# Kernel optimization log

Measured on AMD Instinct MI355X. Metric: run time of the kernel, lower is better.

The kernel has to match this reference:

```python
import jax, jax.numpy as jnp
import numpy as np

SCALE_WEIGHT = 0.5 ** 0.5


def setup_inputs() -> dict:
    key = jax.random.key(0)
    ks = jax.random.split(key, 6)
    B, C, T, S = 8, 512, 2048, 2048
    base_target_emb = jax.random.normal(ks[0], (B, C, T, 1), dtype=jnp.float32)
    inp = jax.random.normal(ks[1], (B, C, T, 1), dtype=jnp.float32)
    encoder_out_t = jax.random.normal(ks[2], (B, C, S), dtype=jnp.float32)
    encoder_out_c = jax.random.normal(ks[3], (B, C, S), dtype=jnp.float32)
    # nn.Linear(input_size, input_size) params: W [out, in], b [out]
    bound = 1.0 / np.sqrt(C)
    W = jax.random.uniform(ks[4], (C, C), minval=-bound, maxval=bound, dtype=jnp.float32)
    b = jax.random.uniform(ks[5], (C,), minval=-bound, maxval=bound, dtype=jnp.float32)
    return {"base_target_emb": base_target_emb, "input": inp,
            "encoder_out_t": encoder_out_t, "encoder_out_c": encoder_out_c,
            "W": W, "b": b}


def reference(base_target_emb, input, encoder_out_t, encoder_out_c, W, b):
    # base_target_emb, input: [B, C, T, 1]; encoder_out_t/c: [B, C, S]
    x = input[..., 0]                                   # [B, C, T]
    # seq_linear: Linear over channel dim (y = W x + b)
    preatt = jnp.einsum('bct,oc->bot', x, W) + b[None, :, None]
    target = (base_target_emb[..., 0] + preatt) * SCALE_WEIGHT  # [B, C, T]
    # bmm(target^T, enc_t): scores over source positions
    pre_a = jnp.einsum('bct,bcs->bts', target, encoder_out_t)   # [B, T, S]
    attn = jax.nn.softmax(pre_a, axis=-1)                       # [B, T, S]
    # bmm(attn, enc_c^T): attention-weighted sum of values
    ctx = jnp.einsum('bts,bcs->btc', attn, encoder_out_c)       # [B, T, C]
    context_output = jnp.transpose(ctx, (0, 2, 1))[..., None]   # [B, C, T, 1]
    return context_output, attn
```

## Files before the change

### kernel.cpp

```cpp
#include <hip/hip_runtime.h>

typedef unsigned short u16;
typedef __attribute__((ext_vector_type(4))) float f4;
typedef __attribute__((ext_vector_type(8))) short bf8;
typedef __attribute__((ext_vector_type(8))) _Float16 h8;
typedef __attribute__((ext_vector_type(4))) unsigned short u16x4;

#define B_ 8
#define C_ 512
#define T_ 2048
#define S_ 2048
#define SCALE_W 0.70710678118654752440f

__device__ __forceinline__ u16 f2h(float f) {
  return __builtin_bit_cast(u16, (_Float16)f);
}
__device__ __forceinline__ float h2f(u16 h) {
  return (float)__builtin_bit_cast(_Float16, h);
}

__device__ __forceinline__ void gload16(const u16* g, u16* l) {
  __builtin_amdgcn_global_load_lds((__attribute__((address_space(1))) const void*)g,
                                   (__attribute__((address_space(3))) void*)l, 16, 0, 0);
}

#define MEMF() asm volatile("" ::: "memory")
#define BAR()  do { MEMF(); __builtin_amdgcn_s_barrier(); MEMF(); } while (0)
#define LGKM0() do { asm volatile("s_waitcnt lgkmcnt(0)" ::: "memory"); \
                     __builtin_amdgcn_sched_barrier(0); } while (0)

__global__ __launch_bounds__(256) void transpose_kernel(
    const float* __restrict__ in, u16* __restrict__ oh, int X)
{
  __shared__ float t[32][33];
  const int tx = threadIdx.x, ty = threadIdx.y;
  const long cbase = (long)blockIdx.z * C_ + blockIdx.y * 32;
  const long xbase = (long)blockIdx.x * 32;
  const float* ip = in + cbase * X + xbase;
#pragma unroll
  for (int i = 0; i < 4; ++i)
    t[ty + i * 8][tx] = ip[(long)(ty + i * 8) * X + tx];
  __syncthreads();
  const long obase = ((long)blockIdx.z * X + xbase) * C_ + blockIdx.y * 32;
#pragma unroll
  for (int i = 0; i < 4; ++i)
    oh[obase + (long)(ty + i * 8) * C_ + tx] = f2h(t[tx][ty + i * 8]);
}

template<int LO>
__global__ __launch_bounds__(256) void split_kernel(
    const float* __restrict__ in, u16* __restrict__ oh, u16* __restrict__ ol, long n4)
{
  long i = (long)blockIdx.x * 256 + threadIdx.x;
  const long stride = (long)gridDim.x * 256;
  for (; i < n4; i += stride) {
    f4 v = ((const f4*)in)[i];
    u16x4 hv, lv;
#pragma unroll
    for (int j = 0; j < 4; ++j) {
      u16 h = f2h(v[j]);
      hv[j] = h;
      if (LO) lv[j] = f2h(v[j] - h2f(h));
    }
    ((u16x4*)oh)[i] = hv;
    if (LO) ((u16x4*)ol)[i] = lv;
  }
}

__global__ __launch_bounds__(256, 2) void gemm1_kernel(
    const u16* __restrict__ A,
    const u16* __restrict__ Bh, const u16* __restrict__ Bl,
    const float* __restrict__ baseO, const float* __restrict__ bias,
    u16* __restrict__ outH, u16* __restrict__ outL)
{
  constexpr int BM = 128, BK = 32, K = C_, N = C_;
  constexpr int TILE = BM * BK;
  __shared__ u16 lA[TILE], lBh[TILE], lBl[TILE];

  const int tid = threadIdx.x;
  const int wid = tid >> 6;
  const int lane = tid & 63;
  const int wr = wid >> 1, wc = wid & 1;
  const int bz = blockIdx.z;
  const int m0 = blockIdx.y * BM;
  const int n0 = blockIdx.x * BM;

  const u16* gA  = A + ((long)bz * T_ + m0) * K;
  const u16* gBh = Bh + (long)n0 * K;
  const u16* gBl = Bl + (long)n0 * K;

  const int srow = tid >> 2;
  const int skoff = (tid & 3) * 8;
  const int ldsOff = wid * 512;

  f4 acc[4][4] = {};

  for (int k0 = 0; k0 < K; k0 += BK) {
    __syncthreads();
#pragma unroll
    for (int c = 0; c < 2; ++c) {
      const long go = (long)(c * 64 + srow) * K + k0 + skoff;
      const int lo = c * 2048 + ldsOff;
      gload16(gA + go, lA + lo);
      gload16(gBh + go, lBh + lo);
      gload16(gBl + go, lBl + lo);
    }
    asm volatile("s_waitcnt vmcnt(0)" ::: "memory");
    __syncthreads();

    bf8 a_[4], b_h[4], b_l[4];
    const int fr = lane & 15;
    const int fk = (lane >> 4) * 8;
#pragma unroll
    for (int i = 0; i < 4; ++i) {
      a_[i]  = *(const bf8*)&lA[(wr * 64 + i * 16 + fr) * BK + fk];
      b_h[i] = *(const bf8*)&lBh[(wc * 64 + i * 16 + fr) * BK + fk];
      b_l[i] = *(const bf8*)&lBl[(wc * 64 + i * 16 + fr) * BK + fk];
    }
#pragma unroll
    for (int mi = 0; mi < 4; ++mi)
#pragma unroll
      for (int ni = 0; ni < 4; ++ni) {
        acc[mi][ni] = __builtin_amdgcn_mfma_f32_16x16x32_f16(
            __builtin_bit_cast(h8, a_[mi]), __builtin_bit_cast(h8, b_h[ni]),
            acc[mi][ni], 0, 0, 0);
        acc[mi][ni] = __builtin_amdgcn_mfma_f32_16x16x32_f16(
            __builtin_bit_cast(h8, a_[mi]), __builtin_bit_cast(h8, b_l[ni]),
            acc[mi][ni], 0, 0, 0);
      }
  }

  const int fr = lane & 15;
  const int r4 = (lane >> 4) * 4;
#pragma unroll
  for (int mi = 0; mi < 4; ++mi) {
#pragma unroll
    for (int ni = 0; ni < 4; ++ni) {
      const int gn = n0 + wc * 64 + ni * 16 + fr;
      const long gmb = m0 + wr * 64 + mi * 16 + r4;
      f4 bv = *(const f4*)(baseO + ((long)bz * C_ + gn) * T_ + gmb);
      const float bs = bias[gn];
#pragma unroll
      for (int r = 0; r < 4; ++r) {
        float val = (acc[mi][ni][r] + bv[r] + bs) * SCALE_W;
        const long idx = ((long)bz * T_ + gmb + r) * (long)N + gn;
        u16 h = f2h(val);
        outH[idx] = h;
        outL[idx] = f2h(val - h2f(h));
      }
    }
  }
}

template<int NT, int TPP, int LDK>
__device__ __forceinline__ void stage2(const u16* g, u16* l) {
  gload16(g, l);
  gload16(g + 64 * LDK, l + 4096);
}
template<int NF>
__device__ __forceinline__ void rd_frags(bf8 (&d)[NF][2], const u16* p, int k0o, int k1o) {
#pragma unroll
  for (int i = 0; i < NF; ++i) {
    d[i][0] = *(const bf8*)&p[i * 1024 + k0o];
    d[i][1] = *(const bf8*)&p[i * 1024 + k1o];
  }
}
template<int MH, int NH>
__device__ __forceinline__ void mmq(f4 (&acc)[8][4], const bf8 (&a)[4][2], const bf8 (&b)[2][2]) {
  __builtin_amdgcn_s_setprio(1);
#pragma unroll
  for (int mi = 0; mi < 4; ++mi)
#pragma unroll
    for (int ni = 0; ni < 2; ++ni)
#pragma unroll
      for (int ks = 0; ks < 2; ++ks)
        acc[MH * 4 + mi][NH * 2 + ni] = __builtin_amdgcn_mfma_f32_16x16x32_f16(
            __builtin_bit_cast(h8, a[mi][ks]), __builtin_bit_cast(h8, b[ni][ks]),
            acc[MH * 4 + mi][NH * 2 + ni], 0, 0, 0);
  __builtin_amdgcn_s_setprio(0);
}

template<int NT, int TPP, int LDK>
__global__ __launch_bounds__(512, 2) void gemm8p_kernel(
    const u16* __restrict__ A0, const u16* __restrict__ A1,
    const u16* __restrict__ B0,
    float* __restrict__ outF,
    long sA, long sB, long sO, int Nr)
{
  __shared__ u16 lds[65536];
  const int tid = threadIdx.x;
  const int wid = tid >> 6, lane = tid & 63;
  const int wr = wid >> 2, wc = wid & 3;

  const int gx = gridDim.x, gy = gridDim.y;
  int lin = blockIdx.x + gx * (blockIdx.y + gy * blockIdx.z);
  const int nwg = gx * gy * (int)gridDim.z;
  lin = (lin & 7) * (nwg >> 3) + (lin >> 3);
  const int bx = lin % gx;
  const int tmp = lin / gx;
  const int by = tmp % gy, bz = tmp / gy;

  const int m0 = by * 256, n0 = bx * 256;
  const u16* gA0 = A0 + (long)bz * sA + (long)m0 * LDK;
  const u16* gA1 = A1 + (long)bz * sA + (long)m0 * LDK;
  const u16* gB  = B0 + (long)bz * sB + (long)n0 * LDK;

  const int srow = tid >> 3;
  const int scol = (((tid & 7) ^ (srow & 7)) * 8);
  const int dstA = tid * 8;

  const int fr = lane & 15;
  const int k0o = (((lane >> 4) ^ (lane & 7)) * 8);
  const int k1o = k0o ^ 32;
  const int abase = (wr * 128 + fr) * 64;
  const int bbase = 32768 + (wc * 64 + fr) * 64;

  f4 acc[8][4] = {};

#define SRC_A(tt) ((((tt) / TPP) == 0 ? gA0 : gA1) + ((tt) % TPP) * 64)
#define SRC_B(tt) (gB + ((tt) % TPP) * 64)
#define STAGE_A(tt, h) stage2<NT, TPP, LDK>(SRC_A(tt) + (long)((h) * 128 + srow) * LDK + scol, \
                              lds + (((tt) & 1) * 16384 + (h) * 8192 + dstA))
#define STAGE_B(tt, h) stage2<NT, TPP, LDK>(SRC_B(tt) + (long)((h) * 128 + srow) * LDK + scol, \
                              lds + (32768 + ((tt) & 1) * 16384 + (h) * 8192 + dstA))

  STAGE_B(0, 0); STAGE_B(0, 1); STAGE_A(0, 0); STAGE_A(0, 1); STAGE_B(1, 0);
  asm volatile("s_waitcnt vmcnt(2)" ::: "memory");
  BAR();

  bf8 af[4][2], b0[2][2], b1[2][2];
  for (int kt = 0; kt < NT - 1; ++kt) {
    const int cur = kt & 1;
    const u16* la = lds + cur * 16384 + abase;
    const u16* lb = lds + cur * 16384 + bbase;
    rd_frags(af, la, k0o, k1o);
    rd_frags(b0, lb, k0o, k1o);
    STAGE_B(kt + 1, 1);
    BAR(); LGKM0();
    mmq<0, 0>(acc, af, b0);
    BAR();
    rd_frags(b1, lb + 2048, k0o, k1o);
    STAGE_A(kt + 1, 0);
    BAR(); LGKM0();
    mmq<0, 1>(acc, af, b1);
    BAR();
    rd_frags(af, la + 4096, k0o, k1o);
    STAGE_A(kt + 1, 1);
    BAR(); LGKM0();
    mmq<1, 0>(acc, af, b0);
    BAR();
    {
      int t2 = kt + 2; if (t2 > NT - 1) t2 = NT - 1;
      STAGE_B(t2, 0);
    }
    BAR();
    mmq<1, 1>(acc, af, b1);
    if (kt == NT - 2) { asm volatile("s_waitcnt vmcnt(0)" ::: "memory"); }
    else             { asm volatile("s_waitcnt vmcnt(2)" ::: "memory"); }
    BAR();
  }
  {
    const int cur = (NT - 1) & 1;
    const u16* la = lds + cur * 16384 + abase;
    const u16* lb = lds + cur * 16384 + bbase;
    rd_frags(af, la, k0o, k1o);
    rd_frags(b0, lb, k0o, k1o);
    BAR(); LGKM0();
    mmq<0, 0>(acc, af, b0);
    BAR();
    rd_frags(b1, lb + 2048, k0o, k1o);
    BAR(); LGKM0();
    mmq<0, 1>(acc, af, b1);
    BAR();
    rd_frags(af, la + 4096, k0o, k1o);
    BAR(); LGKM0();
    mmq<1, 0>(acc, af, b0);
    BAR();
    mmq<1, 1>(acc, af, b1);
  }
#undef SRC_A
#undef SRC_B
#undef STAGE_A
#undef STAGE_B

  const int r4 = (lane >> 4) * 4;
#pragma unroll
  for (int am = 0; am < 8; ++am) {
#pragma unroll
    for (int an = 0; an < 4; ++an) {
      const long gm = m0 + wr * 128 + am * 16 + r4;
      const int gn = n0 + wc * 64 + an * 16 + fr;
      float* po = outF + (long)bz * sO + gm * (long)Nr + gn;
#pragma unroll
      for (int r = 0; r < 4; ++r) po[(long)r * Nr] = acc[am][an][r];
    }
  }
}

__global__ __launch_bounds__(256) void softmax_kernel(float* __restrict__ a,
                                                      u16* __restrict__ ab) {
  const int tid = threadIdx.x;
  float* p = a + (long)blockIdx.x * 2048;
  u16* pb = ab + (long)blockIdx.x * 2048;
  f4 v0 = ((const f4*)p)[tid];
  f4 v1 = ((const f4*)p)[tid + 256];
  float m = fmaxf(fmaxf(fmaxf(v0[0], v0[1]), fmaxf(v0[2], v0[3])),
                  fmaxf(fmaxf(v1[0], v1[1]), fmaxf(v1[2], v1[3])));
#pragma unroll
  for (int o = 32; o >= 1; o >>= 1) m = fmaxf(m, __shfl_xor(m, o));
  __shared__ float redm[4], reds[4];
  if ((tid & 63) == 0) redm[tid >> 6] = m;
  __syncthreads();
  m = fmaxf(fmaxf(redm[0], redm[1]), fmaxf(redm[2], redm[3]));
  float s = 0.f;
#pragma unroll
  for (int j = 0; j < 4; ++j) { v0[j] = __expf(v0[j] - m); s += v0[j]; }
#pragma unroll
  for (int j = 0; j < 4; ++j) { v1[j] = __expf(v1[j] - m); s += v1[j]; }
#pragma unroll
  for (int o = 32; o >= 1; o >>= 1) s += __shfl_xor(s, o);
  if ((tid & 63) == 0) reds[tid >> 6] = s;
  __syncthreads();
  const float inv = 1.0f / (reds[0] + reds[1] + reds[2] + reds[3]);
  v0 *= inv; v1 *= inv;
  ((f4*)p)[tid] = v0;
  ((f4*)p)[tid + 256] = v1;
  u16x4 c0, c1;
#pragma unroll
  for (int j = 0; j < 4; ++j) { c0[j] = f2h(v0[j]); c1[j] = f2h(v1[j]); }
  ((u16x4*)pb)[tid] = c0;
  ((u16x4*)pb)[tid + 256] = c1;
}

extern "C" void kernel_launch(void* const* d_in, const int* in_sizes, int n_in,
                              void* d_out, int out_size, void* d_ws, size_t ws_size,
                              hipStream_t stream) {
  const float* base  = (const float*)d_in[0];
  const float* x     = (const float*)d_in[1];
  const float* enc_t = (const float*)d_in[2];
  const float* enc_c = (const float*)d_in[3];
  const float* W     = (const float*)d_in[4];
  const float* bias  = (const float*)d_in[5];

  float* ctx  = (float*)d_out;
  float* attn = ctx + (long)B_ * C_ * T_;

  const long NBTC = (long)B_ * T_ * C_;
  u16* x_h  = (u16*)d_ws;
  u16* et_h = x_h + NBTC;
  u16* ec_h = x_h + 4 * NBTC;
  u16* w_h  = ec_h + NBTC;
  u16* w_l  = w_h + (long)C_ * C_;

  u16* t_h = (u16*)d_out;
  u16* t_l = t_h + NBTC;
  u16* attn_h = x_h;

  dim3 tb(32, 8);
  transpose_kernel<<<dim3(T_ / 32, C_ / 32, B_), tb, 0, stream>>>(x, x_h, T_);
  transpose_kernel<<<dim3(S_ / 32, C_ / 32, B_), tb, 0, stream>>>(enc_t, et_h, S_);
  split_kernel<0><<<2048, 256, 0, stream>>>(enc_c, ec_h, nullptr, (long)B_ * C_ * S_ / 4);
  split_kernel<1><<<256, 256, 0, stream>>>(W, w_h, w_l, (long)C_ * C_ / 4);

  gemm1_kernel<<<dim3(C_ / 128, T_ / 128, B_), 256, 0, stream>>>(
      x_h, w_h, w_l, base, bias, t_h, t_l);

  gemm8p_kernel<16, 8, 512><<<dim3(S_ / 256, T_ / 256, B_), 512, 0, stream>>>(
      t_h, t_l, et_h, attn,
      (long)T_ * C_, (long)S_ * C_, (long)T_ * S_, S_);

  softmax_kernel<<<B_ * T_, 256, 0, stream>>>(attn, attn_h);

  gemm8p_kernel<32, 32, 2048><<<dim3(T_ / 256, C_ / 256, B_), 512, 0, stream>>>(
      ec_h, ec_h, attn_h, ctx,
      (long)C_ * S_, (long)T_ * S_, (long)C_ * T_, T_);

  (void)in_sizes; (void)n_in; (void)out_size; (void)ws_size;
}
```

Before: 263.7 us.

## Store pre-softmax scores as fp16 and use 128-row tiles for context GEMM

The score GEMM now writes fp16 pre-softmax logits to a workspace buffer. Softmax reads those fp16 values, writes the fp32 attention output, and overwrites the buffer in place with fp16 probabilities, which removes a full fp32 read-write round trip of the large score matrix. The context GEMM is templated to a 128-row M tile (MF=2), doubling its grid from 128 to 256 workgroups for better CU coverage on a small M dimension. The cost is reduced logit precision, since fp16 rounding of the scores before softmax may perturb the attention output.

```diff
diff --git a/kernel.cpp b/kernel.cpp
--- a/kernel.cpp
+++ b/kernel.cpp
@@ -152,8 +152,13 @@
   }
 }
 
-template<int NT, int TPP, int LDK>
-__device__ __forceinline__ void stage2(const u16* g, u16* l) {
+template<int MF, int LDK>
+__device__ __forceinline__ void stage_a(const u16* g, u16* l) {
+  gload16(g, l);
+  if (MF == 4) gload16(g + 64 * LDK, l + 4096);
+}
+template<int LDK>
+__device__ __forceinline__ void stage_b(const u16* g, u16* l) {
   gload16(g, l);
   gload16(g + 64 * LDK, l + 4096);
 }
@@ -165,29 +170,30 @@
     d[i][1] = *(const bf8*)&p[i * 1024 + k1o];
   }
 }
-template<int MH, int NH>
-__device__ __forceinline__ void mmq(f4 (&acc)[8][4], const bf8 (&a)[4][2], const bf8 (&b)[2][2]) {
+template<int MH, int NH, int MF>
+__device__ __forceinline__ void mmq(f4 (&acc)[2 * MF][4], const bf8 (&a)[MF][2],
+                                    const bf8 (&b)[2][2]) {
   __builtin_amdgcn_s_setprio(1);
 #pragma unroll
-  for (int mi = 0; mi < 4; ++mi)
+  for (int mi = 0; mi < MF; ++mi)
 #pragma unroll
     for (int ni = 0; ni < 2; ++ni)
 #pragma unroll
       for (int ks = 0; ks < 2; ++ks)
-        acc[MH * 4 + mi][NH * 2 + ni] = __builtin_amdgcn_mfma_f32_16x16x32_f16(
+        acc[MH * MF + mi][NH * 2 + ni] = __builtin_amdgcn_mfma_f32_16x16x32_f16(
             __builtin_bit_cast(h8, a[mi][ks]), __builtin_bit_cast(h8, b[ni][ks]),
-            acc[MH * 4 + mi][NH * 2 + ni], 0, 0, 0);
+            acc[MH * MF + mi][NH * 2 + ni], 0, 0, 0);
   __builtin_amdgcn_s_setprio(0);
 }
 
-template<int NT, int TPP, int LDK>
+template<int NT, int TPP, int LDK, int MF, int OUT16>
 __global__ __launch_bounds__(512, 2) void gemm8p_kernel(
     const u16* __restrict__ A0, const u16* __restrict__ A1,
     const u16* __restrict__ B0,
-    float* __restrict__ outF,
+    void* __restrict__ outP,
     long sA, long sB, long sO, int Nr)
 {
-  __shared__ u16 lds[65536];
+  __shared__ u16 lds[MF * 8192 + 32768];
   const int tid = threadIdx.x;
   const int wid = tid >> 6, lane = tid & 63;
   const int wr = wid >> 2, wc = wid & 3;
@@ -200,7 +206,7 @@
   const int tmp = lin / gx;
   const int by = tmp % gy, bz = tmp / gy;
 
-  const int m0 = by * 256, n0 = bx * 256;
+  const int m0 = by * (MF * 64), n0 = bx * 256;
   const u16* gA0 = A0 + (long)bz * sA + (long)m0 * LDK;
   const u16* gA1 = A1 + (long)bz * sA + (long)m0 * LDK;
   const u16* gB  = B0 + (long)bz * sB + (long)n0 * LDK;
@@ -212,71 +218,73 @@
   const int fr = lane & 15;
   const int k0o = (((lane >> 4) ^ (lane & 7)) * 8);
   const int k1o = k0o ^ 32;
-  const int abase = (wr * 128 + fr) * 64;
-  const int bbase = 32768 + (wc * 64 + fr) * 64;
-
-  f4 acc[8][4] = {};
+  const int abase = (wr * (MF * 32) + fr) * 64;
+  const int bbase = MF * 8192 + (wc * 64 + fr) * 64;
+
+  f4 acc[2 * MF][4] = {};
 
 #define SRC_A(tt) ((((tt) / TPP) == 0 ? gA0 : gA1) + ((tt) % TPP) * 64)
 #define SRC_B(tt) (gB + ((tt) % TPP) * 64)
-#define STAGE_A(tt, h) stage2<NT, TPP, LDK>(SRC_A(tt) + (long)((h) * 128 + srow) * LDK + scol, \
-                              lds + (((tt) & 1) * 16384 + (h) * 8192 + dstA))
-#define STAGE_B(tt, h) stage2<NT, TPP, LDK>(SRC_B(tt) + (long)((h) * 128 + srow) * LDK + scol, \
-                              lds + (32768 + ((tt) & 1) * 16384 + (h) * 8192 + dstA))
+#define STAGE_A(tt, h) stage_a<MF, LDK>( \
+    SRC_A(tt) + (long)((h) * (MF * 32) + srow) * LDK + scol, \
+    lds + (((tt) & 1) * (MF * 4096) + (h) * (MF * 2048) + dstA))
+#define STAGE_B(tt, h) stage_b<LDK>( \
+    SRC_B(tt) + (long)((h) * 128 + srow) * LDK + scol, \
+    lds + (MF * 8192 + ((tt) & 1) * 16384 + (h) * 8192 + dstA))
 
   STAGE_B(0, 0); STAGE_B(0, 1); STAGE_A(0, 0); STAGE_A(0, 1); STAGE_B(1, 0);
   asm volatile("s_waitcnt vmcnt(2)" ::: "memory");
   BAR();
 
-  bf8 af[4][2], b0[2][2], b1[2][2];
+  bf8 af[MF][2], b0[2][2], b1[2][2];
   for (int kt = 0; kt < NT - 1; ++kt) {
     const int cur = kt & 1;
-    const u16* la = lds + cur * 16384 + abase;
+    const u16* la = lds + cur * (MF * 4096) + abase;
     const u16* lb = lds + cur * 16384 + bbase;
     rd_frags(af, la, k0o, k1o);
     rd_frags(b0, lb, k0o, k1o);
     STAGE_B(kt + 1, 1);
     BAR(); LGKM0();
-    mmq<0, 0>(acc, af, b0);
+    mmq<0, 0, MF>(acc, af, b0);
     BAR();
     rd_frags(b1, lb + 2048, k0o, k1o);
     STAGE_A(kt + 1, 0);
     BAR(); LGKM0();
-    mmq<0, 1>(acc, af, b1);
-    BAR();
-    rd_frags(af, la + 4096, k0o, k1o);
+    mmq<0, 1, MF>(acc, af, b1);
+    BAR();
+    rd_frags(af, la + MF * 1024, k0o, k1o);
     STAGE_A(kt + 1, 1);
     BAR(); LGKM0();
-    mmq<1, 0>(acc, af, b0);
+    mmq<1, 0, MF>(acc, af, b0);
     BAR();
     {
       int t2 = kt + 2; if (t2 > NT - 1) t2 = NT - 1;
       STAGE_B(t2, 0);
     }
     BAR();
-    mmq<1, 1>(acc, af, b1);
+    mmq<1, 1, MF>(acc, af, b1);
     if (kt == NT - 2) { asm volatile("s_waitcnt vmcnt(0)" ::: "memory"); }
     else             { asm volatile("s_waitcnt vmcnt(2)" ::: "memory"); }
     BAR();
   }
   {
     const int cur = (NT - 1) & 1;
-    const u16* la = lds + cur * 16384 + abase;
+    const u16* la = lds + cur * (MF * 4096) + abase;
     const u16* lb = lds + cur * 16384 + bbase;
     rd_frags(af, la, k0o, k1o);
     rd_frags(b0, lb, k0o, k1o);
     BAR(); LGKM0();
-    mmq<0, 0>(acc, af, b0);
+    mmq<0, 0, MF>(acc, af, b0);
     BAR();
     rd_frags(b1, lb + 2048, k0o, k1o);
     BAR(); LGKM0();
-    mmq<0, 1>(acc, af, b1);
-    BAR();
-    rd_frags(af, la + 4096, k0o, k1o);
-    BAR(); LGKM0();
-    mmq<1, 0>(acc, af, b0);
-    BAR();
-    mmq<1, 1>(acc, af, b1);
+    mmq<0, 1, MF>(acc, af, b1);
+    BAR();
+    rd_frags(af, la + MF * 1024, k0o, k1o);
+    BAR(); LGKM0();
+    mmq<1, 0, MF>(acc, af, b0);
+    BAR();
+    mmq<1, 1, MF>(acc, af, b1);
   }
 #undef SRC_A
 #undef SRC_B
@@ -285,25 +293,34 @@
 
   const int r4 = (lane >> 4) * 4;
 #pragma unroll
-  for (int am = 0; am < 8; ++am) {
+  for (int am = 0; am < 2 * MF; ++am) {
 #pragma unroll
     for (int an = 0; an < 4; ++an) {
-      const long gm = m0 + wr * 128 + am * 16 + r4;
+      const long gm = m0 + wr * (MF * 32) + am * 16 + r4;
       const int gn = n0 + wc * 64 + an * 16 + fr;
-      float* po = outF + (long)bz * sO + gm * (long)Nr + gn;
-#pragma unroll
-      for (int r = 0; r < 4; ++r) po[(long)r * Nr] = acc[am][an][r];
-    }
-  }
-}
-
-__global__ __launch_bounds__(256) void softmax_kernel(float* __restrict__ a,
-                                                      u16* __restrict__ ab) {
+      if (OUT16) {
+        u16* po = (u16*)outP + (long)bz * sO + gm * (long)Nr + gn;
+#pragma unroll
+        for (int r = 0; r < 4; ++r) po[(long)r * Nr] = f2h(acc[am][an][r]);
+      } else {
+        float* po = (float*)outP + (long)bz * sO + gm * (long)Nr + gn;
+#pragma unroll
+        for (int r = 0; r < 4; ++r) po[(long)r * Nr] = acc[am][an][r];
+      }
+    }
+  }
+}
+
+__global__ __launch_bounds__(256) void softmax_kernel(u16* __restrict__ pah,
+                                                      float* __restrict__ aout) {
   const int tid = threadIdx.x;
-  float* p = a + (long)blockIdx.x * 2048;
-  u16* pb = ab + (long)blockIdx.x * 2048;
-  f4 v0 = ((const f4*)p)[tid];
-  f4 v1 = ((const f4*)p)[tid + 256];
+  u16* ph = pah + (long)blockIdx.x * 2048;
+  float* pf = aout + (long)blockIdx.x * 2048;
+  u16x4 h0 = ((const u16x4*)ph)[tid];
+  u16x4 h1 = ((const u16x4*)ph)[tid + 256];
+  f4 v0, v1;
+#pragma unroll
+  for (int j = 0; j < 4; ++j) { v0[j] = h2f(h0[j]); v1[j] = h2f(h1[j]); }
   float m = fmaxf(fmaxf(fmaxf(v0[0], v0[1]), fmaxf(v0[2], v0[3])),
                   fmaxf(fmaxf(v1[0], v1[1]), fmaxf(v1[2], v1[3])));
 #pragma unroll
@@ -323,13 +340,12 @@
   __syncthreads();
   const float inv = 1.0f / (reds[0] + reds[1] + reds[2] + reds[3]);
   v0 *= inv; v1 *= inv;
-  ((f4*)p)[tid] = v0;
-  ((f4*)p)[tid + 256] = v1;
-  u16x4 c0, c1;
-#pragma unroll
-  for (int j = 0; j < 4; ++j) { c0[j] = f2h(v0[j]); c1[j] = f2h(v1[j]); }
-  ((u16x4*)pb)[tid] = c0;
-  ((u16x4*)pb)[tid + 256] = c1;
+  ((f4*)pf)[tid] = v0;
+  ((f4*)pf)[tid + 256] = v1;
+#pragma unroll
+  for (int j = 0; j < 4; ++j) { h0[j] = f2h(v0[j]); h1[j] = f2h(v1[j]); }
+  ((u16x4*)ph)[tid] = h0;
+  ((u16x4*)ph)[tid + 256] = h1;
 }
 
 extern "C" void kernel_launch(void* const* d_in, const int* in_sizes, int n_in,
@@ -346,15 +362,16 @@
   float* attn = ctx + (long)B_ * C_ * T_;
 
   const long NBTC = (long)B_ * T_ * C_;
-  u16* x_h  = (u16*)d_ws;
-  u16* et_h = x_h + NBTC;
-  u16* ec_h = x_h + 4 * NBTC;
-  u16* w_h  = ec_h + NBTC;
+  u16* ws   = (u16*)d_ws;
+  u16* x_h  = ws;
+  u16* et_h = ws + NBTC;
+  u16* pre  = ws + 2 * NBTC;
+  u16* ec_h = ws + 6 * NBTC;
+  u16* w_h  = ws + 7 * NBTC;
   u16* w_l  = w_h + (long)C_ * C_;
 
   u16* t_h = (u16*)d_out;
   u16* t_l = t_h + NBTC;
-  u16* attn_h = x_h;
 
   dim3 tb(32, 8);
   transpose_kernel<<<dim3(T_ / 32, C_ / 32, B_), tb, 0, stream>>>(x, x_h, T_);
@@ -365,14 +382,14 @@
   gemm1_kernel<<<dim3(C_ / 128, T_ / 128, B_), 256, 0, stream>>>(
       x_h, w_h, w_l, base, bias, t_h, t_l);
 
-  gemm8p_kernel<16, 8, 512><<<dim3(S_ / 256, T_ / 256, B_), 512, 0, stream>>>(
-      t_h, t_l, et_h, attn,
+  gemm8p_kernel<16, 8, 512, 4, 1><<<dim3(S_ / 256, T_ / 256, B_), 512, 0, stream>>>(
+      t_h, t_l, et_h, pre,
       (long)T_ * C_, (long)S_ * C_, (long)T_ * S_, S_);
 
-  softmax_kernel<<<B_ * T_, 256, 0, stream>>>(attn, attn_h);
-
-  gemm8p_kernel<32, 32, 2048><<<dim3(T_ / 256, C_ / 256, B_), 512, 0, stream>>>(
-      ec_h, ec_h, attn_h, ctx,
+  softmax_kernel<<<B_ * T_, 256, 0, stream>>>(pre, attn);
+
+  gemm8p_kernel<32, 32, 2048, 2, 0><<<dim3(T_ / 256, C_ / 128, B_), 512, 0, stream>>>(
+      ec_h, ec_h, pre, ctx,
       (long)C_ * S_, (long)T_ * S_, (long)C_ * T_, T_);
 
   (void)in_sizes; (void)n_in; (void)out_size; (void)ws_size;
```

Measured after the change: 244.2 us. 1.08x faster.
